# Kernel tuning notes

Measured on AMD Instinct MI355X. Metric: run time of the kernel, lower is better.

Reference implementation:

```python
import jax, jax.numpy as jnp
import numpy as np

NUM_EXPERTS = 16
TOPK = 2
NUM_SHARED = 2


def setup_inputs() -> dict:
    key = jax.random.key(0)
    k1, k2, k3, k4 = jax.random.split(key, 4)
    B, S, D = 4, 2048, 1024
    feat = jax.random.normal(k1, (B, S, D), dtype=jnp.float32)
    router_w = jax.random.normal(k2, (NUM_EXPERTS, D), dtype=jnp.float32) * 0.02
    shared_w = jax.random.normal(k3, (NUM_SHARED * D, D), dtype=jnp.float32) * 0.02
    expert_w = jax.random.normal(k4, (NUM_EXPERTS, D, D), dtype=jnp.float32) * 0.02
    return {"feat": feat, "router_w": router_w, "shared_w": shared_w, "expert_w": expert_w}


def reference(feat, router_w, shared_w, expert_w):
    B, S, D = feat.shape
    T = B * S
    x = feat.reshape(T, D)

    # router logits [T, E]
    logits = x @ router_w.T

    # shared experts: Linear(D, ns*D) then sum over the ns chunks
    shared = (x @ shared_w.T).reshape(T, NUM_SHARED, D).sum(axis=1)

    # gate_topk with norm_probs=True: top-k logits then softmax over them
    topk_vals, topk_idx = jax.lax.top_k(logits, TOPK)       # [T, k]
    weights = jax.nn.softmax(topk_vals, axis=-1)            # [T, k]

    # balance loss (training, token-level): fi = counts/(B*S), pi = mean softmax
    scores = jax.nn.softmax(logits, axis=-1)                # [T, E]
    counts = jnp.zeros((NUM_EXPERTS,), jnp.float32).at[topk_idx.reshape(-1)].add(1.0)
    fi = counts / T
    pi = scores.mean(axis=0)
    aux_loss = jnp.sum(pi * fi)

    # dense combine-weight matrix gate[t,e] = sum_k weights[t,k] * 1[idx[t,k]==e]
    gate = jnp.zeros((T, NUM_EXPERTS), jnp.float32).at[
        jnp.arange(T)[:, None], topk_idx
    ].add(weights)

    # all-expert compute then weighted combine (dense-MoE reference)
    # expert_out[t,e,h] = sum_d x[t,d] * expert_w[e,h,d]
    expert_out = jnp.einsum('td,ehd->teh', x, expert_w)
    moe = jnp.einsum('te,teh->th', gate, expert_out)

    out = (shared + moe).reshape(B, S, D)
    return out, aux_loss
```

## Files before the change

kernel.cpp:

```cpp
#include <hip/hip_runtime.h>
#include <stdint.h>

#define T_TOK 8192
#define DDIM  1024
#define NEXP  16
#define MAXT  208

typedef unsigned short u16;
typedef __attribute__((ext_vector_type(8))) short v8s;
typedef __attribute__((ext_vector_type(4))) float v4f;

__device__ __forceinline__ u16 f2bf(float f) {
  union { float f; unsigned u; } v; v.f = f;
  unsigned r = v.u + 0x7fffu + ((v.u >> 16) & 1u);
  return (u16)(r >> 16);
}

__device__ __forceinline__ void gload_lds16(const u16* gsrc, u16* ldst) {
  typedef __attribute__((address_space(1))) const void GV;
  typedef __attribute__((address_space(3))) void LV;
  __builtin_amdgcn_global_load_lds((GV*)(uintptr_t)gsrc, (LV*)(uintptr_t)ldst, 16, 0, 0);
}

__global__ __launch_bounds__(256) void k_cvt4(const float4* __restrict__ in,
                                              ushort4* __restrict__ out, int n4) {
  int i = blockIdx.x * 256 + threadIdx.x;
  if (i >= n4) return;
  float4 v = in[i];
  ushort4 o; o.x = f2bf(v.x); o.y = f2bf(v.y); o.z = f2bf(v.z); o.w = f2bf(v.w);
  out[i] = o;
}

__global__ __launch_bounds__(256) void k_cvt_shared(const float4* __restrict__ sw,
                                                    ushort4* __restrict__ out, int n4) {
  int i = blockIdx.x * 256 + threadIdx.x;
  if (i >= n4) return;
  float4 a = sw[i];
  float4 b = sw[i + n4];
  ushort4 o;
  o.x = f2bf(a.x + b.x); o.y = f2bf(a.y + b.y);
  o.z = f2bf(a.z + b.z); o.w = f2bf(a.w + b.w);
  out[i] = o;
}

__global__ __launch_bounds__(256) void k_router(const float* __restrict__ x,
                                                const float* __restrict__ rw,
                                                int* __restrict__ topkI,
                                                float* __restrict__ topkW,
                                                int* __restrict__ counts,
                                                float* __restrict__ piSum) {
  __shared__ float lds_pi[NEXP];
  __shared__ int   lds_cnt[NEXP];
  int tid = threadIdx.x;
  if (tid < NEXP) { lds_pi[tid] = 0.f; lds_cnt[tid] = 0; }
  __syncthreads();
  int lane = tid & 63, wave = tid >> 6;

  for (int ti = 0; ti < 8; ++ti) {
    int t = blockIdx.x * 32 + wave * 8 + ti;
    const float* xr = x + (size_t)t * DDIM;
    float xv[16];
#pragma unroll
    for (int i = 0; i < 16; ++i) xv[i] = xr[i * 64 + lane];
    float lg[NEXP];
#pragma unroll
    for (int e = 0; e < NEXP; ++e) {
      const float* wr = rw + (size_t)e * DDIM;
      float p = 0.f;
#pragma unroll
      for (int i = 0; i < 16; ++i) p += xv[i] * wr[i * 64 + lane];
#pragma unroll
      for (int off = 32; off > 0; off >>= 1) p += __shfl_xor(p, off);
      lg[e] = p;
    }
    float mx = lg[0];
#pragma unroll
    for (int e = 1; e < NEXP; ++e) mx = fmaxf(mx, lg[e]);
    float sum = 0.f;
#pragma unroll
    for (int e = 0; e < NEXP; ++e) sum += __expf(lg[e] - mx);
    float v0 = lg[0]; int i0 = 0;
#pragma unroll
    for (int e = 1; e < NEXP; ++e) if (lg[e] > v0) { v0 = lg[e]; i0 = e; }
    float v1 = -3.0e38f; int i1 = 0;
#pragma unroll
    for (int e = 0; e < NEXP; ++e) if (e != i0 && lg[e] > v1) { v1 = lg[e]; i1 = e; }
    float e1 = __expf(v1 - v0);
    float w0 = 1.f / (1.f + e1);
    float w1 = e1 / (1.f + e1);
    if (lane == 0) {
      topkI[2 * t] = i0; topkI[2 * t + 1] = i1;
      topkW[2 * t] = w0; topkW[2 * t + 1] = w1;
      atomicAdd(&lds_cnt[i0], 1); atomicAdd(&lds_cnt[i1], 1);
    }
#pragma unroll
    for (int e = 0; e < NEXP; ++e)
      if (lane == e) atomicAdd(&lds_pi[e], __expf(lg[e] - mx) / sum);
  }
  __syncthreads();
  if (tid < NEXP) {
    atomicAdd(&counts[tid], lds_cnt[tid]);
    atomicAdd(&piSum[tid], lds_pi[tid]);
  }
}

__global__ void k_finalize(const int* __restrict__ counts, const float* __restrict__ piSum,
                           int* __restrict__ offs, int* __restrict__ meta,
                           int* __restrict__ ntile, int* __restrict__ cursor,
                           float* __restrict__ outAux) {
  if (threadIdx.x != 0) return;
  int off = 0;
  for (int e = 0; e < NEXP; ++e) { offs[e] = off; off += counts[e]; }
  offs[NEXP] = off;
  int nt = 0;
  for (int rs = 0; rs < T_TOK; rs += 128) { meta[2 * nt] = NEXP; meta[2 * nt + 1] = rs; ++nt; }
  for (int e = 0; e < NEXP; ++e) {
    for (int rs = 0; rs < counts[e]; rs += 128) { meta[2 * nt] = e; meta[2 * nt + 1] = rs; ++nt; }
    cursor[e] = 0;
  }
  ntile[0] = nt;
  float aux = 0.f;
  for (int e = 0; e < NEXP; ++e)
    aux += (piSum[e] / (float)T_TOK) * ((float)counts[e] / (float)T_TOK);
  outAux[0] = aux;
}

__global__ __launch_bounds__(256) void k_scatter(const int* __restrict__ topkI,
                                                 const float* __restrict__ topkW,
                                                 const int* __restrict__ offs,
                                                 int* __restrict__ cursor,
                                                 int* __restrict__ rowTok,
                                                 float* __restrict__ rowW) {
  __shared__ int lcnt[NEXP], lbase[NEXP];
  int tid = threadIdx.x;
  if (tid < NEXP) lcnt[tid] = 0;
  __syncthreads();
  int p = blockIdx.x * 256 + tid;
  int e = topkI[p];
  int myLocal = atomicAdd(&lcnt[e], 1);
  __syncthreads();
  if (tid < NEXP) lbase[tid] = atomicAdd(&cursor[tid], lcnt[tid]);
  __syncthreads();
  int dst = offs[e] + lbase[e] + myLocal;
  rowTok[dst] = p >> 1;
  rowW[dst] = topkW[p];
}

__global__ __launch_bounds__(256, 4) void k_gemm(const u16* __restrict__ xb,
                                                 const u16* __restrict__ wb,
                                                 const int* __restrict__ meta,
                                                 const int* __restrict__ ntile,
                                                 const int* __restrict__ offs,
                                                 const int* __restrict__ rowTok,
                                                 const float* __restrict__ rowW,
                                                 float* __restrict__ out) {
  __shared__ u16 As[2][4096];
  __shared__ u16 Bs[2][4096];
  int tid = threadIdx.x;
  int ti = blockIdx.x;
  if (ti >= ntile[0]) return;
  int lane = tid & 63, wave = tid >> 6;
  int tileN = blockIdx.y;

  int e = meta[2 * ti], rowStart = meta[2 * ti + 1];
  int offBase = 0, cnt;
  int srow = tid & 127;
  int kc8 = (tid >> 7) * 8;
  int tok;
  if (e == NEXP) {
    cnt = T_TOK; tok = rowStart + srow;
  } else {
    offBase = offs[e]; cnt = offs[e + 1] - offBase;
    tok = rowTok[offBase + min(rowStart + srow, cnt - 1)];
  }
  const u16* aRow = xb + (size_t)tok * DDIM + kc8;
  const u16* bRow = wb + (size_t)e * (DDIM * DDIM) + (size_t)(tileN * 128 + srow) * DDIM + kc8;

  v4f acc[4][4];
#pragma unroll
  for (int m = 0; m < 4; ++m)
#pragma unroll
    for (int n = 0; n < 4; ++n) acc[m][n] = (v4f)0.f;

  int wm = (wave >> 1) * 64, wn = (wave & 1) * 64;
  int rsel = lane & 15;
  int q = lane >> 4;

#define STAGE(buf, k0)                                              \
  do {                                                              \
    gload_lds16(aRow + (k0),      &As[buf][wave * 512]);            \
    gload_lds16(aRow + (k0) + 16, &As[buf][2048 + wave * 512]);     \
    gload_lds16(bRow + (k0),      &Bs[buf][wave * 512]);            \
    gload_lds16(bRow + (k0) + 16, &Bs[buf][2048 + wave * 512]);     \
  } while (0)

  STAGE(0, 0);
  __syncthreads();

  int cur = 0;
  for (int t = 0; t < DDIM / 32; ++t) {
    if (t + 1 < DDIM / 32) STAGE(cur ^ 1, (t + 1) * 32);

    v8s af[4], bfr[4];
#pragma unroll
    for (int m = 0; m < 4; ++m)
      af[m] = *(const v8s*)&As[cur][(q * 128 + wm + m * 16 + rsel) * 8];
#pragma unroll
    for (int n = 0; n < 4; ++n)
      bfr[n] = *(const v8s*)&Bs[cur][(q * 128 + wn + n * 16 + rsel) * 8];
#pragma unroll
    for (int m = 0; m < 4; ++m)
#pragma unroll
      for (int n = 0; n < 4; ++n)
        acc[m][n] = __builtin_amdgcn_mfma_f32_16x16x32_bf16(af[m], bfr[n], acc[m][n], 0, 0, 0);

    __syncthreads();
    cur ^= 1;
  }
#undef STAGE

  int colBase = tileN * 128 + wn + rsel;
#pragma unroll
  for (int m = 0; m < 4; ++m) {
    int rloc = rowStart + wm + m * 16 + q * 4;
#pragma unroll
    for (int j = 0; j < 4; ++j) {
      int r = rloc + j;
      if (r < cnt) {
        int t; float w;
        if (e == NEXP) { t = r; w = 1.f; }
        else { t = rowTok[offBase + r]; w = rowW[offBase + r]; }
        float* orow = out + (size_t)t * DDIM;
#pragma unroll
        for (int n = 0; n < 4; ++n)
          atomicAdd(orow + colBase + n * 16, w * acc[m][n][j]);
      }
    }
  }
}

extern "C" void kernel_launch(void* const* d_in, const int* in_sizes, int n_in,
                              void* d_out, int out_size, void* d_ws, size_t ws_size,
                              hipStream_t stream) {
  const float* feat = (const float*)d_in[0];
  const float* rw   = (const float*)d_in[1];
  const float* sw   = (const float*)d_in[2];
  const float* ew   = (const float*)d_in[3];
  float* out = (float*)d_out;
  char* ws = (char*)d_ws;

  u16* xb = (u16*)(ws + 0);
  u16* wb = (u16*)(ws + 16777216);
  char* smallBase = ws + 52428800;
  int*   counts = (int*)(smallBase + 0);
  float* piSum  = (float*)(smallBase + 64);
  int*   cursor = (int*)(smallBase + 128);
  int*   ntile  = (int*)(smallBase + 192);
  int*   topkI  = (int*)(ws + 52429056);
  float* topkW  = (float*)(ws + 52494592);
  int*   offs   = (int*)(ws + 52560128);
  int*   rowTok = (int*)(ws + 52560256);
  float* rowW   = (float*)(ws + 52625792);
  int*   meta   = (int*)(ws + 52691328);

  hipMemsetAsync(smallBase, 0, 256, stream);
  hipMemsetAsync(out, 0, (size_t)out_size * sizeof(float), stream);

  k_cvt4<<<8192, 256, 0, stream>>>((const float4*)feat, (ushort4*)xb, 2097152);
  k_cvt4<<<16384, 256, 0, stream>>>((const float4*)ew, (ushort4*)wb, 4194304);
  k_cvt_shared<<<1024, 256, 0, stream>>>((const float4*)sw,
                                         (ushort4*)(wb + (size_t)NEXP * DDIM * DDIM), 262144);

  k_router<<<256, 256, 0, stream>>>(feat, rw, topkI, topkW, counts, piSum);
  k_finalize<<<1, 64, 0, stream>>>(counts, piSum, offs, meta, ntile, cursor, out + 8388608);
  k_scatter<<<64, 256, 0, stream>>>(topkI, topkW, offs, cursor, rowTok, rowW);

  dim3 gFused(MAXT, 8);
  k_gemm<<<gFused, 256, 0, stream>>>(xb, wb, meta, ntile, offs, rowTok, rowW, out);
}
```

Baseline: 403.8 us.

## Pre-tile bf16 operands into k-chunk-major layouts and reorder gemm grid

```diff
diff --git a/kernel.cpp b/kernel.cpp
--- a/kernel.cpp
+++ b/kernel.cpp
@@ -4,7 +4,7 @@
 #define T_TOK 8192
 #define DDIM  1024
 #define NEXP  16
-#define MAXT  208
+#define MAXTI 208
 
 typedef unsigned short u16;
 typedef __attribute__((ext_vector_type(8))) short v8s;
@@ -22,25 +22,44 @@
   __builtin_amdgcn_global_load_lds((GV*)(uintptr_t)gsrc, (LV*)(uintptr_t)ldst, 16, 0, 0);
 }
 
-__global__ __launch_bounds__(256) void k_cvt4(const float4* __restrict__ in,
-                                              ushort4* __restrict__ out, int n4) {
-  int i = blockIdx.x * 256 + threadIdx.x;
-  if (i >= n4) return;
-  float4 v = in[i];
-  ushort4 o; o.x = f2bf(v.x); o.y = f2bf(v.y); o.z = f2bf(v.z); o.w = f2bf(v.w);
-  out[i] = o;
-}
-
-__global__ __launch_bounds__(256) void k_cvt_shared(const float4* __restrict__ sw,
-                                                    ushort4* __restrict__ out, int n4) {
-  int i = blockIdx.x * 256 + threadIdx.x;
-  if (i >= n4) return;
-  float4 a = sw[i];
-  float4 b = sw[i + n4];
-  ushort4 o;
-  o.x = f2bf(a.x + b.x); o.y = f2bf(a.y + b.y);
-  o.z = f2bf(a.z + b.z); o.w = f2bf(a.w + b.w);
-  out[i] = o;
+__global__ __launch_bounds__(256) void k_cvtX(const float* __restrict__ feat,
+                                              u16* __restrict__ xbT) {
+  int id = blockIdx.x * 256 + threadIdx.x;
+  int tok = id & 8191, kcg = id >> 13;
+  const float4* s = (const float4*)(feat + (size_t)tok * DDIM + kcg * 8);
+  float4 a = s[0], b = s[1];
+  ushort4 o0 = {f2bf(a.x), f2bf(a.y), f2bf(a.z), f2bf(a.w)};
+  ushort4 o1 = {f2bf(b.x), f2bf(b.y), f2bf(b.z), f2bf(b.w)};
+  ushort4* d = (ushort4*)(xbT + (size_t)id * 8);
+  d[0] = o0; d[1] = o1;
+}
+
+__global__ __launch_bounds__(256) void k_cvtW(const float* __restrict__ ew,
+                                              u16* __restrict__ wt) {
+  int id = blockIdx.x * 256 + threadIdx.x;
+  int row = id & 127, kc = (id >> 7) & 3, kk = (id >> 9) & 31;
+  int tileN = (id >> 14) & 7, e = id >> 17;
+  const float4* s = (const float4*)(ew + (size_t)e * 1048576 +
+                                    (size_t)(tileN * 128 + row) * DDIM + kk * 32 + kc * 8);
+  float4 a = s[0], b = s[1];
+  ushort4 o0 = {f2bf(a.x), f2bf(a.y), f2bf(a.z), f2bf(a.w)};
+  ushort4 o1 = {f2bf(b.x), f2bf(b.y), f2bf(b.z), f2bf(b.w)};
+  ushort4* d = (ushort4*)(wt + (size_t)id * 8);
+  d[0] = o0; d[1] = o1;
+}
+
+__global__ __launch_bounds__(256) void k_cvtS(const float* __restrict__ sw,
+                                              u16* __restrict__ wt) {
+  int id = blockIdx.x * 256 + threadIdx.x;
+  int row = id & 127, kc = (id >> 7) & 3, kk = (id >> 9) & 31, tileN = (id >> 14) & 7;
+  int h = tileN * 128 + row;
+  const float4* s0 = (const float4*)(sw + (size_t)h * DDIM + kk * 32 + kc * 8);
+  const float4* s1 = (const float4*)(sw + (size_t)(1024 + h) * DDIM + kk * 32 + kc * 8);
+  float4 a = s0[0], b = s0[1], c = s1[0], d4 = s1[1];
+  ushort4 o0 = {f2bf(a.x + c.x), f2bf(a.y + c.y), f2bf(a.z + c.z), f2bf(a.w + c.w)};
+  ushort4 o1 = {f2bf(b.x + d4.x), f2bf(b.y + d4.y), f2bf(b.z + d4.z), f2bf(b.w + d4.w)};
+  ushort4* d = (ushort4*)(wt + (size_t)(16 * 131072 + id) * 8);
+  d[0] = o0; d[1] = o1;
 }
 
 __global__ __launch_bounds__(256) void k_router(const float* __restrict__ x,
@@ -105,24 +124,26 @@
 }
 
 __global__ void k_finalize(const int* __restrict__ counts, const float* __restrict__ piSum,
-                           int* __restrict__ offs, int* __restrict__ meta,
-                           int* __restrict__ ntile, int* __restrict__ cursor,
-                           float* __restrict__ outAux) {
-  if (threadIdx.x != 0) return;
-  int off = 0;
-  for (int e = 0; e < NEXP; ++e) { offs[e] = off; off += counts[e]; }
-  offs[NEXP] = off;
-  int nt = 0;
-  for (int rs = 0; rs < T_TOK; rs += 128) { meta[2 * nt] = NEXP; meta[2 * nt + 1] = rs; ++nt; }
-  for (int e = 0; e < NEXP; ++e) {
-    for (int rs = 0; rs < counts[e]; rs += 128) { meta[2 * nt] = e; meta[2 * nt + 1] = rs; ++nt; }
-    cursor[e] = 0;
-  }
-  ntile[0] = nt;
-  float aux = 0.f;
-  for (int e = 0; e < NEXP; ++e)
-    aux += (piSum[e] / (float)T_TOK) * ((float)counts[e] / (float)T_TOK);
-  outAux[0] = aux;
+                           int* __restrict__ offs, int* __restrict__ tileStart,
+                           int* __restrict__ cursor, float* __restrict__ outAux) {
+  int lane = threadIdx.x;
+  int c = (lane < NEXP) ? counts[lane] : 0;
+  float p = (lane < NEXP) ? piSum[lane] : 0.f;
+  int tc = (c + 127) >> 7;
+  int ic = c, itc = tc;
+  for (int d = 1; d < NEXP; d <<= 1) {
+    int v1 = __shfl_up(ic, d), v2 = __shfl_up(itc, d);
+    if (lane >= d) { ic += v1; itc += v2; }
+  }
+  if (lane < NEXP) {
+    offs[lane] = ic - c;
+    tileStart[lane] = 64 + itc - tc;
+    cursor[lane] = 0;
+    if (lane == NEXP - 1) { offs[NEXP] = ic; tileStart[NEXP] = 64 + itc; }
+  }
+  float term = (lane < NEXP) ? (p / (float)T_TOK) * ((float)c / (float)T_TOK) : 0.f;
+  for (int off = 8; off; off >>= 1) term += __shfl_xor(term, off);
+  if (lane == 0) outAux[0] = term;
 }
 
 __global__ __launch_bounds__(256) void k_scatter(const int* __restrict__ topkI,
@@ -146,10 +167,9 @@
   rowW[dst] = topkW[p];
 }
 
-__global__ __launch_bounds__(256, 4) void k_gemm(const u16* __restrict__ xb,
-                                                 const u16* __restrict__ wb,
-                                                 const int* __restrict__ meta,
-                                                 const int* __restrict__ ntile,
+__global__ __launch_bounds__(256, 4) void k_gemm(const u16* __restrict__ xbT,
+                                                 const u16* __restrict__ wt,
+                                                 const int* __restrict__ tileStart,
                                                  const int* __restrict__ offs,
                                                  const int* __restrict__ rowTok,
                                                  const float* __restrict__ rowW,
@@ -157,24 +177,27 @@
   __shared__ u16 As[2][4096];
   __shared__ u16 Bs[2][4096];
   int tid = threadIdx.x;
-  int ti = blockIdx.x;
-  if (ti >= ntile[0]) return;
+  int tileN = blockIdx.x;
+  int ti = blockIdx.y;
+  if (ti >= tileStart[NEXP]) return;
+
+  int e, rowStart, offBase = 0, cnt;
+  if (ti < 64) { e = NEXP; rowStart = ti * 128; cnt = T_TOK; }
+  else {
+    e = 0;
+    while (ti >= tileStart[e + 1]) ++e;
+    rowStart = (ti - tileStart[e]) * 128;
+    offBase = offs[e]; cnt = offs[e + 1] - offBase;
+  }
+
   int lane = tid & 63, wave = tid >> 6;
-  int tileN = blockIdx.y;
-
-  int e = meta[2 * ti], rowStart = meta[2 * ti + 1];
-  int offBase = 0, cnt;
   int srow = tid & 127;
-  int kc8 = (tid >> 7) * 8;
+  int kcLo = tid >> 7;
   int tok;
-  if (e == NEXP) {
-    cnt = T_TOK; tok = rowStart + srow;
-  } else {
-    offBase = offs[e]; cnt = offs[e + 1] - offBase;
-    tok = rowTok[offBase + min(rowStart + srow, cnt - 1)];
-  }
-  const u16* aRow = xb + (size_t)tok * DDIM + kc8;
-  const u16* bRow = wb + (size_t)e * (DDIM * DDIM) + (size_t)(tileN * 128 + srow) * DDIM + kc8;
+  if (e == NEXP) tok = rowStart + srow;
+  else tok = rowTok[offBase + min(rowStart + srow, cnt - 1)];
+  const u16* aBase = xbT + (size_t)tok * 8;
+  const u16* wTile = wt + (size_t)(e * 8 + tileN) * 32 * 4096;
 
   v4f acc[4][4];
 #pragma unroll
@@ -186,20 +209,23 @@
   int rsel = lane & 15;
   int q = lane >> 4;
 
-#define STAGE(buf, k0)                                              \
-  do {                                                              \
-    gload_lds16(aRow + (k0),      &As[buf][wave * 512]);            \
-    gload_lds16(aRow + (k0) + 16, &As[buf][2048 + wave * 512]);     \
-    gload_lds16(bRow + (k0),      &Bs[buf][wave * 512]);            \
-    gload_lds16(bRow + (k0) + 16, &Bs[buf][2048 + wave * 512]);     \
+#define STAGE(buf, kk)                                                          \
+  do {                                                                          \
+    gload_lds16(aBase + (size_t)((kk) * 4 + kcLo) * 65536,                      \
+                &As[buf][wave * 512]);                                          \
+    gload_lds16(aBase + (size_t)((kk) * 4 + kcLo + 2) * 65536,                  \
+                &As[buf][2048 + wave * 512]);                                   \
+    gload_lds16(wTile + (size_t)(kk) * 4096 + tid * 8, &Bs[buf][wave * 512]);   \
+    gload_lds16(wTile + (size_t)(kk) * 4096 + (tid + 256) * 8,                  \
+                &Bs[buf][2048 + wave * 512]);                                   \
   } while (0)
 
   STAGE(0, 0);
   __syncthreads();
 
   int cur = 0;
-  for (int t = 0; t < DDIM / 32; ++t) {
-    if (t + 1 < DDIM / 32) STAGE(cur ^ 1, (t + 1) * 32);
+  for (int t = 0; t < 32; ++t) {
+    if (t + 1 < 32) STAGE(cur ^ 1, t + 1);
 
     v8s af[4], bfr[4];
 #pragma unroll
@@ -249,32 +275,30 @@
   float* out = (float*)d_out;
   char* ws = (char*)d_ws;
 
-  u16* xb = (u16*)(ws + 0);
-  u16* wb = (u16*)(ws + 16777216);
+  u16* xbT = (u16*)(ws + 0);
+  u16* wt  = (u16*)(ws + 16777216);
   char* smallBase = ws + 52428800;
-  int*   counts = (int*)(smallBase + 0);
-  float* piSum  = (float*)(smallBase + 64);
-  int*   cursor = (int*)(smallBase + 128);
-  int*   ntile  = (int*)(smallBase + 192);
-  int*   topkI  = (int*)(ws + 52429056);
-  float* topkW  = (float*)(ws + 52494592);
-  int*   offs   = (int*)(ws + 52560128);
-  int*   rowTok = (int*)(ws + 52560256);
-  float* rowW   = (float*)(ws + 52625792);
-  int*   meta   = (int*)(ws + 52691328);
-
-  hipMemsetAsync(smallBase, 0, 256, stream);
+  int*   counts    = (int*)(smallBase + 0);
+  float* piSum     = (float*)(smallBase + 64);
+  int*   cursor    = (int*)(smallBase + 128);
+  int*   offs      = (int*)(smallBase + 192);
+  int*   tileStart = (int*)(smallBase + 320);
+  int*   topkI  = (int*)(ws + 52429824);
+  float* topkW  = (float*)(ws + 52495360);
+  int*   rowTok = (int*)(ws + 52560896);
+  float* rowW   = (float*)(ws + 52626432);
+
+  hipMemsetAsync(smallBase, 0, 192, stream);
   hipMemsetAsync(out, 0, (size_t)out_size * sizeof(float), stream);
 
-  k_cvt4<<<8192, 256, 0, stream>>>((const float4*)feat, (ushort4*)xb, 2097152);
-  k_cvt4<<<16384, 256, 0, stream>>>((const float4*)ew, (ushort4*)wb, 4194304);
-  k_cvt_shared<<<1024, 256, 0, stream>>>((const float4*)sw,
-                                         (ushort4*)(wb + (size_t)NEXP * DDIM * DDIM), 262144);
+  k_cvtX<<<4096, 256, 0, stream>>>(feat, xbT);
+  k_cvtW<<<8192, 256, 0, stream>>>(ew, wt);
+  k_cvtS<<<512, 256, 0, stream>>>(sw, wt);
 
   k_router<<<256, 256, 0, stream>>>(feat, rw, topkI, topkW, counts, piSum);
-  k_finalize<<<1, 64, 0, stream>>>(counts, piSum, offs, meta, ntile, cursor, out + 8388608);
+  k_finalize<<<1, 64, 0, stream>>>(counts, piSum, offs, tileStart, cursor, out + 8388608);
   k_scatter<<<64, 256, 0, stream>>>(topkI, topkW, offs, cursor, rowTok, rowW);
 
-  dim3 gFused(MAXT, 8);
-  k_gemm<<<gFused, 256, 0, stream>>>(xb, wb, meta, ntile, offs, rowTok, rowW, out);
-}
+  dim3 gGemm(8, MAXTI);
+  k_gemm<<<gGemm, 256, 0, stream>>>(xbT, wt, tileStart, offs, rowTok, rowW, out);
+}
```

Measured after the change: 414.0 us. 1.03x slower.
